# Kernel tuning notes

Hardware: AMD Instinct MI355X
Metric: run time of the kernel (lower is better)

The kernel has to match this reference:

```python
import jax, jax.numpy as jnp
import numpy as np

# --- configuration constants (from conf) ---
FEAT_H, FEAT_W, STRIDE = 32, 110, 16       # KITTI 512x1760 image, stride 16
B, G, NA = 8, 32, 36                       # batch, max GT per image, anchors per location
NUM_CLASSES = 4                            # len(lbls)+1
FG_T, BG_LO, BG_HI, BEST_T = 0.5, 0.0, 0.5, 0.35
L_CLS, L_2D, L_3D = 1.0, 1.0, 1.0          # cls_2d_lambda, bbox_2d_lambda, bbox_3d_lambda


def _locate_anchors(anchors):
    """Tile anchor templates over the feature grid. Returns boxes [A,4], tracker [A]."""
    sx = (jnp.arange(FEAT_W) * STRIDE).astype(jnp.float32)
    sy = (jnp.arange(FEAT_H) * STRIDE).astype(jnp.float32)
    gx, gy = jnp.meshgrid(sx, sy)                              # [H,W]
    shifts = jnp.stack([gx, gy, gx, gy], -1).reshape(-1, 4)    # [H*W,4]
    boxes = shifts[:, None, :] + anchors[None, :, 0:4]         # [H*W,NA,4]
    tracker = jnp.broadcast_to(jnp.arange(NA), (FEAT_H * FEAT_W, NA))
    return boxes.reshape(-1, 4), tracker.reshape(-1)


def _iou(rois, gts):
    # rois [A,4], gts [G,4] -> IoU [A,G]
    x1 = jnp.maximum(rois[:, None, 0], gts[None, :, 0])
    y1 = jnp.maximum(rois[:, None, 1], gts[None, :, 1])
    x2 = jnp.minimum(rois[:, None, 2], gts[None, :, 2])
    y2 = jnp.minimum(rois[:, None, 3], gts[None, :, 3])
    iw = jnp.clip(x2 - x1 + 1.0, 0.0)
    ih = jnp.clip(y2 - y1 + 1.0, 0.0)
    inter = iw * ih
    ar = (rois[:, 2] - rois[:, 0] + 1.0) * (rois[:, 3] - rois[:, 1] + 1.0)
    ag = (gts[:, 2] - gts[:, 0] + 1.0) * (gts[:, 3] - gts[:, 1] + 1.0)
    return inter / (ar[:, None] + ag[None, :] - inter)


def _smooth_l1(x):
    ax = jnp.abs(x)
    return jnp.where(ax < 1.0, 0.5 * ax * ax, ax - 0.5)


def setup_inputs() -> dict:
    key = jax.random.key(0)
    ks = jax.random.split(key, 10)
    A = FEAT_H * FEAT_W * NA
    cls = jax.random.normal(ks[0], (B, A, NUM_CLASSES), jnp.float32)
    bbox_2d = jax.random.normal(ks[1], (B, A, 4), jnp.float32) * 0.1
    bbox_3d = jax.random.normal(ks[2], (B, A, 7), jnp.float32) * 0.1
    # GT 2D boxes inside a 512x1760 image
    x1 = jax.random.uniform(ks[3], (B, G)) * 1500.0
    y1 = jax.random.uniform(ks[4], (B, G)) * 350.0
    w = 30.0 + jax.random.uniform(ks[5], (B, G)) * 200.0
    h = 30.0 + jax.random.uniform(ks[6], (B, G)) * 130.0
    gt_boxes = jnp.stack([x1, y1, x1 + w - 1.0, y1 + h - 1.0], -1)
    # GT 3D: [cx_proj, cy_proj, z, w3d, h3d, l3d, ry]
    k7, k8, k9 = jax.random.split(ks[7], 3)
    z = 5.0 + jax.random.uniform(k7, (B, G)) * 55.0
    dims = 1.0 + jax.random.uniform(k8, (B, G, 3)) * 3.0
    ry = (jax.random.uniform(k9, (B, G)) - 0.5) * (2.0 * np.pi)
    gt_3d = jnp.concatenate([(x1 + w * 0.5)[..., None], (y1 + h * 0.5)[..., None],
                             z[..., None], dims, ry[..., None]], -1)
    gt_labels = jax.random.randint(ks[8], (B, G), 1, NUM_CLASSES)
    gt_valid = jnp.ones((B, G), bool)
    # anchors: [x1,y1,x2,y2, z, w3d, h3d, l3d, ry] (12 scales x 3 aspect ratios)
    scales = np.array([32.0 * (1.26 ** i) for i in range(12)], np.float32)
    ratios = np.array([0.5, 1.0, 1.5], np.float32)
    aw = np.repeat(scales, 3)
    ah = (scales[:, None] * ratios[None, :]).reshape(-1)
    az = np.linspace(60.0, 5.0, NA).astype(np.float32)
    box = np.stack([-(aw - 1) / 2, -(ah - 1) / 2, (aw - 1) / 2, (ah - 1) / 2], -1)
    a3 = np.tile(np.array([1.6, 1.5, 3.9, 0.0], np.float32), (NA, 1))
    anchors = jnp.asarray(np.concatenate([box, az[:, None], a3], -1), jnp.float32)
    bbox_means = jnp.zeros((1, 11), jnp.float32)
    bbox_stds = jnp.concatenate([jnp.full((1, 4), 0.1, jnp.float32),
                                 jnp.full((1, 7), 0.5, jnp.float32)], -1)
    return {"cls": cls, "bbox_2d": bbox_2d, "bbox_3d": bbox_3d,
            "gt_boxes": gt_boxes, "gt_3d": gt_3d, "gt_labels": gt_labels,
            "gt_valid": gt_valid, "anchors": anchors,
            "bbox_means": bbox_means, "bbox_stds": bbox_stds}


def reference(cls, bbox_2d, bbox_3d, gt_boxes, gt_3d, gt_labels, gt_valid,
              anchors, bbox_means, bbox_stds):
    roi_boxes, tracker = _locate_anchors(anchors)          # [A,4], [A]
    widths = roi_boxes[:, 2] - roi_boxes[:, 0] + 1.0
    heights = roi_boxes[:, 3] - roi_boxes[:, 1] + 1.0
    ctr_x = roi_boxes[:, 0] + 0.5 * widths
    ctr_y = roi_boxes[:, 1] + 0.5 * heights
    src = anchors[tracker]                                 # [A,9] per-roi anchor template
    Gn = gt_boxes.shape[1]

    def assign(gtb, gt3, glbl, gval):
        iou = _iou(roi_boxes, gtb)                         # [A,G]
        iou = jnp.where(gval[None, :], iou, -1.0)
        max_ol = iou.max(1)
        agt = iou.argmax(1)                                # assigned GT per anchor
        fg = max_ol >= FG_T
        # best-anchor-per-gt rule (best_thresh)
        gt_best = iou.max(0)
        ba = iou.argmax(0)
        force = gval & (gt_best >= BEST_T)
        fg = fg.at[ba].max(force)
        agt = agt.at[ba].set(jnp.where(force, jnp.arange(Gn), agt[ba]))
        bg = (~fg) & (max_ol < BG_HI) & (max_ol >= BG_LO)  # rest is ignored
        g = gtb[agt]
        g3 = gt3[agt]
        gw = g[:, 2] - g[:, 0] + 1.0
        gh = g[:, 3] - g[:, 1] + 1.0
        gcx = g[:, 0] + 0.5 * gw
        gcy = g[:, 1] + 0.5 * gh
        t2 = jnp.stack([(gcx - ctr_x) / widths, (gcy - ctr_y) / heights,
                        jnp.log(gw / widths), jnp.log(gh / heights)], -1)
        t3 = jnp.stack([(g3[:, 0] - ctr_x) / widths, (g3[:, 1] - ctr_y) / heights,
                        g3[:, 2] - src[:, 4],
                        jnp.log(g3[:, 3] / src[:, 5]),
                        jnp.log(g3[:, 4] / src[:, 6]),
                        jnp.log(g3[:, 5] / src[:, 7]),
                        g3[:, 6] - src[:, 8]], -1)
        t2 = (t2 - bbox_means[0, 0:4]) / bbox_stds[0, 0:4]
        t3 = (t3 - bbox_means[0, 4:11]) / bbox_stds[0, 4:11]
        lbl = jnp.where(fg, glbl[agt], 0)
        return lbl, fg, bg, t2, t3

    lbl, fg, bg, t2, t3 = jax.vmap(assign)(gt_boxes, gt_3d, gt_labels, gt_valid)
    lbl = jax.lax.stop_gradient(lbl)
    t2 = jax.lax.stop_gradient(t2)
    t3 = jax.lax.stop_gradient(t3)
    active = (fg | bg).astype(cls.dtype)
    fgf = fg.astype(cls.dtype)
    logp = jax.nn.log_softmax(cls, -1)
    ce = -jnp.take_along_axis(logp, lbl[..., None], -1)[..., 0]
    n_act = jnp.maximum(active.sum(), 1.0)
    n_fg = jnp.maximum(fgf.sum(), 1.0)
    loss_cls = (ce * active).sum() / n_act
    loss_2d = (_smooth_l1(bbox_2d - t2).sum(-1) * fgf).sum() / n_fg
    loss_3d = (_smooth_l1(bbox_3d - t3).sum(-1) * fgf).sum() / n_fg
    return L_CLS * loss_cls + L_2D * loss_2d + L_3D * loss_3d
```

## Files before the change

### kernel.cpp

```cpp
#include <hip/hip_runtime.h>

#define FEAT_H 32
#define FEAT_W 110
#define NCELL (FEAT_H * FEAT_W)
#define STRIDEPX 16
#define NB 8
#define NG 32
#define NANC 36
#define NC 4
#define A_TOTAL (NCELL * NANC)

#define CPB 576

#define BLK 512
#define CHK 512
#define NCHK 248
#define G2 512
#define CB (G2 / NB)
#define MAXSLOTS 4

__device__ __forceinline__ float smooth_l1(float x) {
    float ax = fabsf(x);
    return ax < 1.f ? 0.5f * ax * ax : ax - 0.5f;
}



__global__ __launch_bounds__(CPB) void k_colpass(
    const float* __restrict__ gt_boxes, const int* __restrict__ gt_valid,
    const float* __restrict__ anchors, unsigned long long* __restrict__ colpart,
    float* __restrict__ acc, unsigned* __restrict__ done) {
#pragma clang fp contract(off)
    __shared__ unsigned long long cand[NANC];
    const int tid = threadIdx.x;
    const int bg = blockIdx.x;
    if (bg == 0) {
        if (tid < 8) acc[tid] = 0.f;
        if (tid == 8) *done = 0u;
    }
    const int t = tid >> 4;
    const int lane = tid & 15;
    const int valid = gt_valid[bg];
    const float g0 = gt_boxes[bg * 4 + 0], g1 = gt_boxes[bg * 4 + 1];
    const float g2 = gt_boxes[bg * 4 + 2], g3 = gt_boxes[bg * 4 + 3];
    const float ag = (g2 - g0 + 1.f) * (g3 - g1 + 1.f);
    const float* ap = anchors + t * 9;
    const float ax0 = ap[0], ay0 = ap[1], ax1 = ap[2], ay1 = ap[3];
    const float aarea = (ax1 - ax0 + 1.f) * (ay1 - ay0 + 1.f);

    float iwm = -1.f; int icol = 0;
    for (int col = lane; col < FEAT_W; col += 16) {
        const float sx = (float)(col * STRIDEPX);
        const float r0 = sx + ax0, r2 = sx + ax1;
        const float xx1 = fmaxf(r0, g0), xx2 = fminf(r2, g2);
        const float iw = fmaxf(xx2 - xx1 + 1.f, 0.f);
        if (iw > iwm) { iwm = iw; icol = col; }
    }
    float ihm = -1.f; int irow = 0;
    for (int row = lane; row < FEAT_H; row += 16) {
        const float sy = (float)(row * STRIDEPX);
        const float r1 = sy + ay0, r3 = sy + ay1;
        const float yy1 = fmaxf(r1, g1), yy2 = fminf(r3, g3);
        const float ih = fmaxf(yy2 - yy1 + 1.f, 0.f);
        if (ih > ihm) { ihm = ih; irow = row; }
    }
    for (int off = 8; off; off >>= 1) {
        const float ow = __shfl_down(iwm, off, 16);
        const int oc = __shfl_down(icol, off, 16);
        if (ow > iwm || (ow == iwm && oc < icol)) { iwm = ow; icol = oc; }
        const float oh = __shfl_down(ihm, off, 16);
        const int orw = __shfl_down(irow, off, 16);
        if (oh > ihm || (oh == ihm && orw < irow)) { ihm = oh; irow = orw; }
    }
    if (lane == 0) {
        const float inter = iwm * ihm;
        const float iou = inter * __builtin_amdgcn_rcpf(aarea + ag - inter);
        const int a = (irow * FEAT_W + icol) * NANC + t;
        cand[t] = valid
            ? (((unsigned long long)__float_as_uint(iou) << 32) |
               (unsigned long long)(0xFFFFFFFFu - (unsigned)a))
            : 0ull;
    }
    __syncthreads();
    if (tid == 0) {
        unsigned long long best = cand[0];
        for (int u = 1; u < NANC; ++u)
            if (cand[u] > best) best = cand[u];
        colpart[bg] = best;
    }
}

__global__ __launch_bounds__(BLK) void k_main(
    const float* __restrict__ cls, const float* __restrict__ bbox_2d,
    const float* __restrict__ bbox_3d, const float* __restrict__ gt_boxes,
    const float* __restrict__ gt_3d, const int* __restrict__ gt_labels,
    const int* __restrict__ gt_valid, const float* __restrict__ anchors,
    const float* __restrict__ means, const float* __restrict__ stds,
    const unsigned long long* __restrict__ colpart, float* __restrict__ acc,
    unsigned* __restrict__ done, float* __restrict__ out) {
#pragma clang fp contract(off)
    __shared__ float ax0_s[NANC], ay0_s[NANC], ax1_s[NANC], ay1_s[NANC];
    __shared__ float anch9[NANC * 9];
    __shared__ float4 gtb4_s[NG];
    __shared__ float gt3_s[NG * 7];
    __shared__ int lbl_s[NG];
    __shared__ int bag_s[NG], forceg_s[NG];
    __shared__ float mean_s[11], rstd_s[11];
    __shared__ unsigned vmask_s;
    __shared__ float red[5][BLK / 64];
    __shared__ int fixmap[MAXSLOTS * BLK];
    __shared__ unsigned fglist[MAXSLOTS * BLK];
    __shared__ int nloc;

    const int tid = threadIdx.x;
    const int b = blockIdx.x / CB;
    const int c0 = blockIdx.x % CB;

    for (int i = tid; i < NANC * 9; i += BLK) anch9[i] = anchors[i];
    if (tid < NANC) {
        const float* ap = anchors + tid * 9;
        ax0_s[tid] = ap[0]; ay0_s[tid] = ap[1];
        ax1_s[tid] = ap[2]; ay1_s[tid] = ap[3];
    }
    for (int i = tid; i < NG * 7; i += BLK) gt3_s[i] = gt_3d[b * NG * 7 + i];
    if (tid == 0) nloc = 0;
    int myval = 0;
    if (tid < NG) {
        const float4 q = ((const float4*)gt_boxes)[b * NG + tid];
        gtb4_s[tid] = q;
        lbl_s[tid] = gt_labels[b * NG + tid];
        myval = gt_valid[b * NG + tid];
        const unsigned long long p = colpart[b * NG + tid];
        const float gbest = __uint_as_float((unsigned)(p >> 32));
        bag_s[tid] = myval ? (int)(0xFFFFFFFFu - (unsigned)(p & 0xFFFFFFFFull)) : 0;
        forceg_s[tid] = (myval && gbest >= 0.35f) ? 1 : 0;
    }
    unsigned long long bal = __ballot(tid < NG && myval);
    if (tid == 0) vmask_s = (unsigned)bal;
    if (tid < 11) { mean_s[tid] = means[tid]; rstd_s[tid] = 1.0f / stds[tid]; }
    for (int i = tid; i < MAXSLOTS * BLK; i += BLK) fixmap[i] = -1;
    __syncthreads();
    if (tid == 0) {
        for (int g = 0; g < NG; ++g) {
            const int ba = bag_s[g];
            const int cb = ba >> 9;
            if (cb % CB == c0) {
                const int k = (cb - c0) / CB;
                const int idx = k * BLK + (ba & (CHK - 1));
                const int e = fixmap[idx];
                const int anyf = ((e >= 0) ? (e & 0x40000000) : 0) |
                                 (forceg_s[g] ? 0x40000000 : 0);
                const int code = forceg_s[g] ? g : 32;
                fixmap[idx] = anyf | code;
            }
        }
    }
    __syncthreads();
    const unsigned vmask = vmask_s;
    const size_t bbase = (size_t)b * A_TOTAL;

    float r0a[MAXSLOTS], r1a[MAXSLOTS], r2a[MAXSLOTS], r3a[MAXSLOTS];
    float ara[MAXSLOTS];
#pragma unroll
    for (int k = 0; k < MAXSLOTS; ++k) {
        const int araw = (c0 + k * CB) * CHK + tid;
        const int ae = araw < A_TOTAL ? araw : (A_TOTAL - 1);
        const int t = ae % NANC;
        const int cell = ae / NANC;
        const float sx = (float)((cell % FEAT_W) * STRIDEPX);
        const float sy = (float)((cell / FEAT_W) * STRIDEPX);
        r0a[k] = sx + ax0_s[t]; r1a[k] = sy + ay0_s[t];
        r2a[k] = sx + ax1_s[t]; r3a[k] = sy + ay1_s[t];
        ara[k] = (r2a[k] - r0a[k] + 1.f) * (r3a[k] - r1a[k] + 1.f);
    }

    const float4* gtb = (const float4*)gt_boxes + (size_t)b * NG;
    float m[MAXSLOTS];
    int ia[MAXSLOTS];
#pragma unroll
    for (int k = 0; k < MAXSLOTS; ++k) { m[k] = -1.f; ia[k] = 0; }
    float4 qn = gtb[0];
#pragma unroll 4
    for (int g = 0; g < NG; ++g) {
        const float4 q = qn;
        if (g + 1 < NG) qn = gtb[g + 1];
        const bool gv = (vmask >> g) & 1u;
        const float agv = (q.z - q.x + 1.f) * (q.w - q.y + 1.f);
#pragma unroll
        for (int k = 0; k < MAXSLOTS; ++k) {
            const float xx1 = fmaxf(r0a[k], q.x), yy1 = fmaxf(r1a[k], q.y);
            const float xx2 = fminf(r2a[k], q.z), yy2 = fminf(r3a[k], q.w);
            const float iw = fmaxf(xx2 - xx1 + 1.f, 0.f);
            const float ih = fmaxf(yy2 - yy1 + 1.f, 0.f);
            const float inter = iw * ih;
            float iou = inter * __builtin_amdgcn_rcpf(ara[k] + agv - inter);
            iou = gv ? iou : -1.0f;
            if (iou > m[k]) { m[k] = iou; ia[k] = g; }
        }
    }

    float4 cvk[MAXSLOTS];
#pragma unroll
    for (int k = 0; k < MAXSLOTS; ++k) {
        const int araw = (c0 + k * CB) * CHK + tid;
        const int ae = araw < A_TOTAL ? araw : (A_TOTAL - 1);
        cvk[k] = *(const float4*)(cls + (bbase + ae) * NC);
    }
    float sum_ce = 0.f, sum_act = 0.f, sum_fg = 0.f, sum_2d = 0.f, sum_3d = 0.f;
#pragma unroll
    for (int k = 0; k < MAXSLOTS; ++k) {
        const bool live = ((c0 + k * CB) * CHK + tid) < A_TOTAL;
        const float best = m[k];
        int agt = ia[k];
        bool fg = best >= 0.5f;
        const int f = fixmap[k * BLK + tid];
        if (f >= 0) {
            if (f & 0x40000000) fg = true;
            const int code = f & 63;
            agt = (code == 32) ? agt : code;
        }
        if (!live) fg = false;
        const bool bgm = live && (!fg) && (best < 0.5f) && (best >= 0.0f);
        const float active = (fg || bgm) ? 1.f : 0.f;
        const int lbl = fg ? lbl_s[agt] : 0;

        const float4 c4 = cvk[k];
        const float mx = fmaxf(fmaxf(c4.x, c4.y), fmaxf(c4.z, c4.w));
        const float se = __expf(c4.x - mx) + __expf(c4.y - mx) +
                         __expf(c4.z - mx) + __expf(c4.w - mx);
        const float lse = mx + __logf(se);
        const float csel = (lbl == 0) ? c4.x : (lbl == 1) ? c4.y
                         : (lbl == 2) ? c4.z : c4.w;
        sum_ce += (lse - csel) * active;
        sum_act += active;

        if (fg) {
            sum_fg += 1.f;
            const int p = atomicAdd(&nloc, 1);
            fglist[p] = ((unsigned)k << 14) | ((unsigned)tid << 5) | (unsigned)agt;
        }
    }

    __syncthreads();
    const int nfgl = nloc;
    for (int i = tid; i < nfgl; i += BLK) {
        const unsigned e = fglist[i];
        const int k2 = (int)(e >> 14);
        const int tid2 = (int)((e >> 5) & 511u);
        const int agt = (int)(e & 31u);
        const int a = (c0 + k2 * CB) * CHK + tid2;
        const int t = a % NANC;
        const int cell = a / NANC;
        const float sx = (float)((cell % FEAT_W) * STRIDEPX);
        const float sy = (float)((cell / FEAT_W) * STRIDEPX);
        const float r0 = sx + ax0_s[t], r1 = sy + ay0_s[t];
        const float r2 = sx + ax1_s[t], r3 = sy + ay1_s[t];
        const float w = r2 - r0 + 1.f, h = r3 - r1 + 1.f;
        const float rw = __builtin_amdgcn_rcpf(w);
        const float rh = __builtin_amdgcn_rcpf(h);
        const float cx = r0 + 0.5f * w, cy = r1 + 0.5f * h;
        const float4 Gq = gtb4_s[agt];
        const float gw = Gq.z - Gq.x + 1.f, gh = Gq.w - Gq.y + 1.f;
        const float gcx = Gq.x + 0.5f * gw, gcy = Gq.y + 0.5f * gh;
        float tt2[4];
        tt2[0] = (gcx - cx) * rw;
        tt2[1] = (gcy - cy) * rh;
        tt2[2] = __logf(gw * rw);
        tt2[3] = __logf(gh * rh);
        const float4 b2 = *(const float4*)(bbox_2d + (bbase + a) * 4);
        const float b2v[4] = {b2.x, b2.y, b2.z, b2.w};
        float l2 = 0.f;
        for (int j = 0; j < 4; ++j)
            l2 += smooth_l1(b2v[j] - (tt2[j] - mean_s[j]) * rstd_s[j]);
        sum_2d += l2;
        const float* q3p = &gt3_s[agt * 7];
        const float* b3 = bbox_3d + (bbase + a) * 7;
        float tt3[7];
        tt3[0] = (q3p[0] - cx) * rw;
        tt3[1] = (q3p[1] - cy) * rh;
        tt3[2] = q3p[2] - anch9[t * 9 + 4];
        tt3[3] = __logf(q3p[3] * __builtin_amdgcn_rcpf(anch9[t * 9 + 5]));
        tt3[4] = __logf(q3p[4] * __builtin_amdgcn_rcpf(anch9[t * 9 + 6]));
        tt3[5] = __logf(q3p[5] * __builtin_amdgcn_rcpf(anch9[t * 9 + 7]));
        tt3[6] = q3p[6] - anch9[t * 9 + 8];
        float l3 = 0.f;
        for (int j = 0; j < 7; ++j)
            l3 += smooth_l1(b3[j] - (tt3[j] - mean_s[4 + j]) * rstd_s[4 + j]);
        sum_3d += l3;
    }

    float vals[5] = {sum_ce, sum_act, sum_fg, sum_2d, sum_3d};
#pragma unroll
    for (int j = 0; j < 5; ++j) {
        float v = vals[j];
        for (int off = 32; off; off >>= 1) v += __shfl_down(v, off, 64);
        if ((tid & 63) == 0) red[j][tid >> 6] = v;
    }
    __syncthreads();
    if (tid == 0) {
        for (int j = 0; j < 5; ++j) {
            float s = 0.f;
            for (int w = 0; w < BLK / 64; ++w) s += red[j][w];
            atomicAdd(&acc[j], s);
        }
        __threadfence();
        const unsigned old = atomicAdd(done, 1u);
        if (old == G2 - 1) {
            const float a0 = atomicAdd(&acc[0], 0.f);
            const float a1 = atomicAdd(&acc[1], 0.f);
            const float a2 = atomicAdd(&acc[2], 0.f);
            const float a3 = atomicAdd(&acc[3], 0.f);
            const float a4 = atomicAdd(&acc[4], 0.f);
            const float nact = fmaxf(a1, 1.f);
            const float nfg = fmaxf(a2, 1.f);
            out[0] = a0 / nact + a3 / nfg + a4 / nfg;
        }
    }
}

extern "C" void kernel_launch(void* const* d_in, const int* in_sizes, int n_in,
                              void* d_out, int out_size, void* d_ws, size_t ws_size,
                              hipStream_t stream) {
    const float* cls      = (const float*)d_in[0];
    const float* bbox_2d  = (const float*)d_in[1];
    const float* bbox_3d  = (const float*)d_in[2];
    const float* gt_boxes = (const float*)d_in[3];
    const float* gt_3d    = (const float*)d_in[4];
    const int*   gt_labels= (const int*)d_in[5];
    const int*   gt_valid = (const int*)d_in[6];
    const float* anchors  = (const float*)d_in[7];
    const float* means    = (const float*)d_in[8];
    const float* stds     = (const float*)d_in[9];

    unsigned long long* colpart = (unsigned long long*)d_ws;
    float* acc = (float*)((char*)d_ws + 8192);
    unsigned* done = (unsigned*)((char*)d_ws + 8192 + 32);
    float* out = (float*)d_out;

    k_colpass<<<NB * NG, CPB, 0, stream>>>(gt_boxes, gt_valid, anchors,
                                           colpart, acc, done);
    k_main<<<G2, BLK, 0, stream>>>(cls, bbox_2d, bbox_3d, gt_boxes, gt_3d,
                                   gt_labels, gt_valid, anchors, means, stds,
                                   colpart, acc, done, out);
}
```

Baseline: 159.8 us.

## Remap anchors so each thread owns one column-anchor across 8 rows

Work is redistributed so each thread handles a fixed (column, anchor template) pair over a group of 8 feature rows. The x-overlap term is computed once per GT and reused across all 8 rows, and the per-slot reciprocal is replaced by a cross-multiplied comparison with a single reciprocal at the end. The grid becomes 31 blocks per image with 8 slots per thread, and fixmap shrinks to short. Classification loads now have a stride of NPAIR between slots rather than being contiguous per block chunk, and more registers are needed per thread.

```diff
diff --git a/kernel.cpp b/kernel.cpp
--- a/kernel.cpp
+++ b/kernel.cpp
@@ -13,11 +13,11 @@
 #define CPB 576
 
 #define BLK 512
-#define CHK 512
-#define NCHK 248
-#define G2 512
-#define CB (G2 / NB)
-#define MAXSLOTS 4
+#define BPI 31
+#define G2 (NB * BPI)
+#define NPAIR 3960
+#define UREAL 15840
+#define NSLOT 8
 
 __device__ __forceinline__ float smooth_l1(float x) {
     float ax = fabsf(x);
@@ -108,13 +108,21 @@
     __shared__ float mean_s[11], rstd_s[11];
     __shared__ unsigned vmask_s;
     __shared__ float red[5][BLK / 64];
-    __shared__ int fixmap[MAXSLOTS * BLK];
-    __shared__ unsigned fglist[MAXSLOTS * BLK];
+    __shared__ short fixmap[NSLOT * BLK];
+    __shared__ unsigned fglist[NSLOT * BLK];
     __shared__ int nloc;
 
     const int tid = threadIdx.x;
-    const int b = blockIdx.x / CB;
-    const int c0 = blockIdx.x % CB;
+    const int blk = blockIdx.x;
+    const int b = blk / BPI;
+    const int ub = (blk % BPI) * BLK;
+    const int u = ub + tid;
+    const bool livet = u < UREAL;
+    const int uc = livet ? u : (UREAL - 1);
+    const int rg = uc / NPAIR;
+    const int p = uc - rg * NPAIR;
+    const int t = p % NANC;
+    const int col = p / NANC;
 
     for (int i = tid; i < NANC * 9; i += BLK) anch9[i] = anchors[i];
     if (tid < NANC) {
@@ -130,28 +138,33 @@
         gtb4_s[tid] = q;
         lbl_s[tid] = gt_labels[b * NG + tid];
         myval = gt_valid[b * NG + tid];
-        const unsigned long long p = colpart[b * NG + tid];
-        const float gbest = __uint_as_float((unsigned)(p >> 32));
-        bag_s[tid] = myval ? (int)(0xFFFFFFFFu - (unsigned)(p & 0xFFFFFFFFull)) : 0;
+        const unsigned long long pk = colpart[b * NG + tid];
+        const float gbest = __uint_as_float((unsigned)(pk >> 32));
+        bag_s[tid] = myval ? (int)(0xFFFFFFFFu - (unsigned)(pk & 0xFFFFFFFFull)) : 0;
         forceg_s[tid] = (myval && gbest >= 0.35f) ? 1 : 0;
     }
     unsigned long long bal = __ballot(tid < NG && myval);
     if (tid == 0) vmask_s = (unsigned)bal;
     if (tid < 11) { mean_s[tid] = means[tid]; rstd_s[tid] = 1.0f / stds[tid]; }
-    for (int i = tid; i < MAXSLOTS * BLK; i += BLK) fixmap[i] = -1;
+    for (int i = tid; i < NSLOT * BLK; i += BLK) fixmap[i] = -1;
     __syncthreads();
     if (tid == 0) {
         for (int g = 0; g < NG; ++g) {
             const int ba = bag_s[g];
-            const int cb = ba >> 9;
-            if (cb % CB == c0) {
-                const int k = (cb - c0) / CB;
-                const int idx = k * BLK + (ba & (CHK - 1));
+            const int t_ = ba % NANC;
+            const int cell = ba / NANC;
+            const int col_ = cell % FEAT_W;
+            const int row_ = cell / FEAT_W;
+            const int pp = col_ * NANC + t_;
+            const int uu = (row_ >> 3) * NPAIR + pp;
+            if ((uu >> 9) == (blk % BPI)) {
+                const int jj = row_ & 7;
+                const int idx = jj * BLK + (uu & (BLK - 1));
                 const int e = fixmap[idx];
-                const int anyf = ((e >= 0) ? (e & 0x40000000) : 0) |
-                                 (forceg_s[g] ? 0x40000000 : 0);
+                const int anyf = ((e >= 0) ? (e & 0x40) : 0) |
+                                 (forceg_s[g] ? 0x40 : 0);
                 const int code = forceg_s[g] ? g : 32;
-                fixmap[idx] = anyf | code;
+                fixmap[idx] = (short)(anyf | code);
             }
         }
     }
@@ -159,26 +172,22 @@
     const unsigned vmask = vmask_s;
     const size_t bbase = (size_t)b * A_TOTAL;
 
-    float r0a[MAXSLOTS], r1a[MAXSLOTS], r2a[MAXSLOTS], r3a[MAXSLOTS];
-    float ara[MAXSLOTS];
+    const float sx = (float)(col * STRIDEPX);
+    const float r0 = sx + ax0_s[t], r2 = sx + ax1_s[t];
+    const float w1 = r2 - r0 + 1.f;
+    float r1a[NSLOT], r3a[NSLOT], ara[NSLOT];
+    float bi[NSLOT], bd[NSLOT];
+    int ia[NSLOT];
 #pragma unroll
-    for (int k = 0; k < MAXSLOTS; ++k) {
-        const int araw = (c0 + k * CB) * CHK + tid;
-        const int ae = araw < A_TOTAL ? araw : (A_TOTAL - 1);
-        const int t = ae % NANC;
-        const int cell = ae / NANC;
-        const float sx = (float)((cell % FEAT_W) * STRIDEPX);
-        const float sy = (float)((cell / FEAT_W) * STRIDEPX);
-        r0a[k] = sx + ax0_s[t]; r1a[k] = sy + ay0_s[t];
-        r2a[k] = sx + ax1_s[t]; r3a[k] = sy + ay1_s[t];
-        ara[k] = (r2a[k] - r0a[k] + 1.f) * (r3a[k] - r1a[k] + 1.f);
+    for (int j = 0; j < NSLOT; ++j) {
+        const float sy = (float)((rg * 8 + j) * STRIDEPX);
+        r1a[j] = sy + ay0_s[t];
+        r3a[j] = sy + ay1_s[t];
+        ara[j] = w1 * (r3a[j] - r1a[j] + 1.f);
+        bi[j] = -1.f; bd[j] = 1.f; ia[j] = 0;
     }
 
     const float4* gtb = (const float4*)gt_boxes + (size_t)b * NG;
-    float m[MAXSLOTS];
-    int ia[MAXSLOTS];
-#pragma unroll
-    for (int k = 0; k < MAXSLOTS; ++k) { m[k] = -1.f; ia[k] = 0; }
     float4 qn = gtb[0];
 #pragma unroll 4
     for (int g = 0; g < NG; ++g) {
@@ -186,45 +195,39 @@
         if (g + 1 < NG) qn = gtb[g + 1];
         const bool gv = (vmask >> g) & 1u;
         const float agv = (q.z - q.x + 1.f) * (q.w - q.y + 1.f);
+        const float xx1 = fmaxf(r0, q.x), xx2 = fminf(r2, q.z);
+        const float iw = fmaxf(xx2 - xx1 + 1.f, 0.f);
 #pragma unroll
-        for (int k = 0; k < MAXSLOTS; ++k) {
-            const float xx1 = fmaxf(r0a[k], q.x), yy1 = fmaxf(r1a[k], q.y);
-            const float xx2 = fminf(r2a[k], q.z), yy2 = fminf(r3a[k], q.w);
-            const float iw = fmaxf(xx2 - xx1 + 1.f, 0.f);
+        for (int j = 0; j < NSLOT; ++j) {
+            const float yy1 = fmaxf(r1a[j], q.y), yy2 = fminf(r3a[j], q.w);
             const float ih = fmaxf(yy2 - yy1 + 1.f, 0.f);
             const float inter = iw * ih;
-            float iou = inter * __builtin_amdgcn_rcpf(ara[k] + agv - inter);
-            iou = gv ? iou : -1.0f;
-            if (iou > m[k]) { m[k] = iou; ia[k] = g; }
-        }
-    }
-
-    float4 cvk[MAXSLOTS];
-#pragma unroll
-    for (int k = 0; k < MAXSLOTS; ++k) {
-        const int araw = (c0 + k * CB) * CHK + tid;
-        const int ae = araw < A_TOTAL ? araw : (A_TOTAL - 1);
-        cvk[k] = *(const float4*)(cls + (bbase + ae) * NC);
-    }
+            const float den = ara[j] + agv - inter;
+            if (gv && inter * bd[j] > bi[j] * den) {
+                bi[j] = inter; bd[j] = den; ia[j] = g;
+            }
+        }
+    }
+
     float sum_ce = 0.f, sum_act = 0.f, sum_fg = 0.f, sum_2d = 0.f, sum_3d = 0.f;
 #pragma unroll
-    for (int k = 0; k < MAXSLOTS; ++k) {
-        const bool live = ((c0 + k * CB) * CHK + tid) < A_TOTAL;
-        const float best = m[k];
-        int agt = ia[k];
+    for (int j = 0; j < NSLOT; ++j) {
+        const float best = bi[j] * __builtin_amdgcn_rcpf(bd[j]);
+        int agt = ia[j];
         bool fg = best >= 0.5f;
-        const int f = fixmap[k * BLK + tid];
+        const int f = fixmap[j * BLK + tid];
         if (f >= 0) {
-            if (f & 0x40000000) fg = true;
+            if (f & 0x40) fg = true;
             const int code = f & 63;
             agt = (code == 32) ? agt : code;
         }
-        if (!live) fg = false;
-        const bool bgm = live && (!fg) && (best < 0.5f) && (best >= 0.0f);
+        if (!livet) fg = false;
+        const bool bgm = livet && (!fg) && (best < 0.5f) && (best >= 0.0f);
         const float active = (fg || bgm) ? 1.f : 0.f;
         const int lbl = fg ? lbl_s[agt] : 0;
 
-        const float4 c4 = cvk[k];
+        const int a = (rg * 8 + j) * NPAIR + p;
+        const float4 c4 = *(const float4*)(cls + (bbase + a) * NC);
         const float mx = fmaxf(fmaxf(c4.x, c4.y), fmaxf(c4.z, c4.w));
         const float se = __expf(c4.x - mx) + __expf(c4.y - mx) +
                          __expf(c4.z - mx) + __expf(c4.w - mx);
@@ -236,8 +239,8 @@
 
         if (fg) {
             sum_fg += 1.f;
-            const int p = atomicAdd(&nloc, 1);
-            fglist[p] = ((unsigned)k << 14) | ((unsigned)tid << 5) | (unsigned)agt;
+            const int q2 = atomicAdd(&nloc, 1);
+            fglist[q2] = ((unsigned)j << 14) | ((unsigned)tid << 5) | (unsigned)agt;
         }
     }
 
@@ -245,20 +248,24 @@
     const int nfgl = nloc;
     for (int i = tid; i < nfgl; i += BLK) {
         const unsigned e = fglist[i];
-        const int k2 = (int)(e >> 14);
+        const int j2 = (int)(e >> 14);
         const int tid2 = (int)((e >> 5) & 511u);
         const int agt = (int)(e & 31u);
-        const int a = (c0 + k2 * CB) * CHK + tid2;
-        const int t = a % NANC;
-        const int cell = a / NANC;
-        const float sx = (float)((cell % FEAT_W) * STRIDEPX);
-        const float sy = (float)((cell / FEAT_W) * STRIDEPX);
-        const float r0 = sx + ax0_s[t], r1 = sy + ay0_s[t];
-        const float r2 = sx + ax1_s[t], r3 = sy + ay1_s[t];
-        const float w = r2 - r0 + 1.f, h = r3 - r1 + 1.f;
+        const int u2 = ub + tid2;
+        const int rg2 = u2 / NPAIR;
+        const int p2 = u2 - rg2 * NPAIR;
+        const int t2 = p2 % NANC;
+        const int col2 = p2 / NANC;
+        const int row2 = rg2 * 8 + j2;
+        const int a = row2 * NPAIR + p2;
+        const float sx2 = (float)(col2 * STRIDEPX);
+        const float sy2 = (float)(row2 * STRIDEPX);
+        const float q0 = sx2 + ax0_s[t2], q1 = sy2 + ay0_s[t2];
+        const float q2_ = sx2 + ax1_s[t2], q3 = sy2 + ay1_s[t2];
+        const float w = q2_ - q0 + 1.f, h = q3 - q1 + 1.f;
         const float rw = __builtin_amdgcn_rcpf(w);
         const float rh = __builtin_amdgcn_rcpf(h);
-        const float cx = r0 + 0.5f * w, cy = r1 + 0.5f * h;
+        const float cx = q0 + 0.5f * w, cy = q1 + 0.5f * h;
         const float4 Gq = gtb4_s[agt];
         const float gw = Gq.z - Gq.x + 1.f, gh = Gq.w - Gq.y + 1.f;
         const float gcx = Gq.x + 0.5f * gw, gcy = Gq.y + 0.5f * gh;
@@ -270,22 +277,22 @@
         const float4 b2 = *(const float4*)(bbox_2d + (bbase + a) * 4);
         const float b2v[4] = {b2.x, b2.y, b2.z, b2.w};
         float l2 = 0.f;
-        for (int j = 0; j < 4; ++j)
-            l2 += smooth_l1(b2v[j] - (tt2[j] - mean_s[j]) * rstd_s[j]);
+        for (int jj = 0; jj < 4; ++jj)
+            l2 += smooth_l1(b2v[jj] - (tt2[jj] - mean_s[jj]) * rstd_s[jj]);
         sum_2d += l2;
         const float* q3p = &gt3_s[agt * 7];
         const float* b3 = bbox_3d + (bbase + a) * 7;
         float tt3[7];
         tt3[0] = (q3p[0] - cx) * rw;
         tt3[1] = (q3p[1] - cy) * rh;
-        tt3[2] = q3p[2] - anch9[t * 9 + 4];
-        tt3[3] = __logf(q3p[3] * __builtin_amdgcn_rcpf(anch9[t * 9 + 5]));
-        tt3[4] = __logf(q3p[4] * __builtin_amdgcn_rcpf(anch9[t * 9 + 6]));
-        tt3[5] = __logf(q3p[5] * __builtin_amdgcn_rcpf(anch9[t * 9 + 7]));
-        tt3[6] = q3p[6] - anch9[t * 9 + 8];
+        tt3[2] = q3p[2] - anch9[t2 * 9 + 4];
+        tt3[3] = __logf(q3p[3] * __builtin_amdgcn_rcpf(anch9[t2 * 9 + 5]));
+        tt3[4] = __logf(q3p[4] * __builtin_amdgcn_rcpf(anch9[t2 * 9 + 6]));
+        tt3[5] = __logf(q3p[5] * __builtin_amdgcn_rcpf(anch9[t2 * 9 + 7]));
+        tt3[6] = q3p[6] - anch9[t2 * 9 + 8];
         float l3 = 0.f;
-        for (int j = 0; j < 7; ++j)
-            l3 += smooth_l1(b3[j] - (tt3[j] - mean_s[4 + j]) * rstd_s[4 + j]);
+        for (int jj = 0; jj < 7; ++jj)
+            l3 += smooth_l1(b3[jj] - (tt3[jj] - mean_s[4 + jj]) * rstd_s[4 + jj]);
         sum_3d += l3;
     }
 
```

Result: faster. 146.1 us (-8.6%).
